# Performance work log

Measured on AMD Instinct MI355X. Metric: run time of the kernel, lower is better.

Reference implementation:

```python
import jax, jax.numpy as jnp
import numpy as np

B, S, H = 2, 2048, 1024
NH, HD = 16, 64
WINDOW = 512
NEG = -10000.0


def setup_inputs() -> dict:
    key = jax.random.key(0)
    ks = jax.random.split(key, 8)
    sc = 0.02
    return {
        "hidden_states": jax.random.normal(ks[0], (B, S, H), dtype=jnp.float32),
        "attention_mask": jnp.zeros((B, 1, 1, S), dtype=jnp.float32),
        "Wq": jax.random.normal(ks[1], (H, H), dtype=jnp.float32) * sc,
        "bq": jnp.zeros((H,), dtype=jnp.float32),
        "Wk": jax.random.normal(ks[2], (H, H), dtype=jnp.float32) * sc,
        "bk": jnp.zeros((H,), dtype=jnp.float32),
        "Wv": jax.random.normal(ks[3], (H, H), dtype=jnp.float32) * sc,
        "bv": jnp.zeros((H,), dtype=jnp.float32),
    }


def _heads(x):
    # [b, t, (h d)] -> [b, h, t, d]
    b, t, _ = x.shape
    return x.reshape(b, t, NH, HD).transpose(0, 2, 1, 3)


def reference(hidden_states, attention_mask, Wq, bq, Wk, bk, Wv, bv):
    q = _heads(hidden_states @ Wq.T + bq)
    k = _heads(hidden_states @ Wk.T + bk)
    v = _heads(hidden_states @ Wv.T + bv)

    # Faithful mask construction (note: window mask is triu(diag=-WINDOW),
    # penalizing the recent window, exactly as in the source).
    i = jnp.arange(S)[:, None]
    j = jnp.arange(S)[None, :]
    causal_mask = jnp.where(j > i, NEG, 0.0).astype(jnp.float32)          # triu, diag=1
    window_mask = jnp.where(j >= i - WINDOW, NEG, 0.0).astype(jnp.float32)  # triu, diag=-512
    mask = causal_mask + window_mask + attention_mask  # [b,1,S,S]

    scale = 1.0 / jnp.sqrt(jnp.asarray(HD, dtype=q.dtype))
    scores = jnp.einsum("bhtd,bhsd->bhts", q, k) * scale + mask  # [b,h,S,S]
    probs = jax.nn.softmax(scores, axis=-1)
    out = jnp.einsum("bhts,bhsd->bhtd", probs, v)  # [b,h,S,d]
    # [b,h,t,d] -> [b,t,(h d)]
    return out.transpose(0, 2, 1, 3).reshape(B, S, H)
```

## Files before the change

### kernel.cpp

```cpp
#include <hip/hip_runtime.h>

typedef float f32x2 __attribute__((ext_vector_type(2)));
typedef float f32x4 __attribute__((ext_vector_type(4)));
typedef float f32x16 __attribute__((ext_vector_type(16)));
typedef _Float16 half8 __attribute__((ext_vector_type(8)));
typedef _Float16 half4 __attribute__((ext_vector_type(4)));
typedef unsigned int u32;
typedef u32 u32x4 __attribute__((ext_vector_type(4)));

#define S_LEN 2048
#define NHEAD 16
#define HDIM 64
#define BATCH 2
#define WINDOW 512
#define M2_FIX 5.770780163555852f
#define LOG2E 1.4426950408889634f

#define GLDS16(gp, lp) __builtin_amdgcn_global_load_lds( \
    (const __attribute__((address_space(1))) void*)(gp), \
    (__attribute__((address_space(3))) void*)(lp), 16, 0, 0)


__global__ __launch_bounds__(256) void convert_kernel(
    const float4* __restrict__ hs, const float4* __restrict__ wq,
    const float4* __restrict__ wk, const float4* __restrict__ wv,
    _Float16* __restrict__ hsb, _Float16* __restrict__ wb) {
  int i = blockIdx.x * 256 + threadIdx.x;
  float4 v;
  _Float16* dst;
  if (i < 1048576) {
    v = hs[i];
    dst = hsb + (size_t)i * 4;
  } else {
    int j = i - 1048576;
    if (j < 262144) v = wq[j];
    else if (j < 524288) v = wk[j - 262144];
    else v = wv[j - 524288];
    dst = wb + (size_t)j * 4;
  }
  half4 o;
  o[0] = (_Float16)v.x; o[1] = (_Float16)v.y;
  o[2] = (_Float16)v.z; o[3] = (_Float16)v.w;
  *(half4*)dst = o;
}

__global__ __launch_bounds__(512) void qkv_gemm(
    const _Float16* __restrict__ A, const _Float16* __restrict__ W,
    const float* __restrict__ bq, const float* __restrict__ bk,
    const float* __restrict__ bv,
    _Float16* __restrict__ Qf, _Float16* __restrict__ Kf, _Float16* __restrict__ Vf) {
  __shared__ _Float16 sbuf[2][24576];
  const int tid = threadIdx.x;
  const int wv = tid >> 6;
  const int lane = tid & 63;
  const int g = lane >> 4;
  const int c = lane & 15;
  const int b = blockIdx.x;
  const int xcd = b & 7;
  const int s = b >> 3;
  const int m0 = ((xcd >> 2) * 8 + (s & 7)) * 256;
  const int n0 = ((xcd & 3) * 6 + (s >> 3)) * 128;
  const int wm = (wv & 3) * 64;
  const int wn = (wv >> 2) * 64;
  const _Float16* Asb0;
  const _Float16* Bsb0;

  const int srow8 = lane >> 3;
  const int sslot = lane & 7;
  const int lsl = sslot ^ srow8;
  const _Float16* aS = A + (size_t)(m0 + wv * 32 + srow8) * 1024 + lsl * 8;
  const _Float16* bS = W + (size_t)(n0 + wv * 16 + srow8) * 1024 + lsl * 8;
  const int aBase = wv * 2048;
  const int bBase = 16384 + wv * 1024;

  f32x4 acc[4][4];
#pragma unroll
  for (int i = 0; i < 4; ++i)
#pragma unroll
    for (int j = 0; j < 4; ++j) acc[i][j] = (f32x4){0.f, 0.f, 0.f, 0.f};

  auto STAGE = [&](int bf_, int k0) __attribute__((always_inline)) {
    char* aD = (char*)&sbuf[bf_][aBase];
    char* bD = (char*)&sbuf[bf_][bBase];
#pragma unroll
    for (int grp = 0; grp < 4; ++grp)
      GLDS16(aS + grp * 8192 + k0, aD + grp * 1024);
#pragma unroll
    for (int grp = 0; grp < 2; ++grp)
      GLDS16(bS + grp * 8192 + k0, bD + grp * 1024);
  };

  STAGE(0, 0);
  __syncthreads();
  int cur = 0;

  for (int t = 0; t < 16; ++t) {
    if (t < 15) STAGE(cur ^ 1, (t + 1) * 64);
    const _Float16* Asb = &sbuf[cur][0];
    const _Float16* Bsb = &sbuf[cur][16384];
    half8 af[4][2];
#pragma unroll
    for (int mf = 0; mf < 4; ++mf) {
      const int row = wm + mf * 16 + c;
#pragma unroll
      for (int ch = 0; ch < 2; ++ch)
        af[mf][ch] = *(const half8*)&Asb[row * 64 + ((ch * 4 + g) ^ (c & 7)) * 8];
    }
#pragma unroll
    for (int nf = 0; nf < 4; ++nf) {
      const int row = wn + nf * 16 + c;
      half8 bf0 = *(const half8*)&Bsb[row * 64 + ((g) ^ (c & 7)) * 8];
      half8 bf1 = *(const half8*)&Bsb[row * 64 + ((4 + g) ^ (c & 7)) * 8];
#pragma unroll
      for (int mf = 0; mf < 4; ++mf) {
        acc[mf][nf] = __builtin_amdgcn_mfma_f32_16x16x32_f16(af[mf][0], bf0, acc[mf][nf], 0, 0, 0);
        acc[mf][nf] = __builtin_amdgcn_mfma_f32_16x16x32_f16(af[mf][1], bf1, acc[mf][nf], 0, 0, 0);
      }
    }
    __syncthreads();
    cur ^= 1;
  }

  const int kind = n0 >> 10;
  const int nb = (n0 + wn) & 1023;
  const int head = nb >> 6;
  const float* bias = kind == 0 ? bq : (kind == 1 ? bk : bv);
  _Float16* dst = kind == 0 ? Qf : (kind == 1 ? Kf : Vf);
  _Float16* ob = &sbuf[0][0] + wv * 4096;

  if (kind < 2) {
    const float scl = kind == 0 ? (0.125f * LOG2E) : 1.0f;
#pragma unroll
    for (int nf = 0; nf < 4; ++nf) {
      const int d = nf * 16 + c;
      const float bsv = bias[nb + d];
      const int base = nf * 512 + ((c >> 3) & 1) * 256 + (c & 7);
#pragma unroll
      for (int mf = 0; mf < 4; ++mf) {
#pragma unroll
        for (int r = 0; r < 4; ++r) {
          ob[(mf >> 1) * 2048 + base + (mf & 1) * 128 + g * 32 + r * 8] =
              (_Float16)((acc[mf][nf][r] + bsv) * scl);
        }
      }
    }
  } else {
#pragma unroll
    for (int nf = 0; nf < 4; ++nf) {
      const int d = nf * 16 + c;
      const float bsv = bias[nb + d];
#pragma unroll
      for (int mf = 0; mf < 4; ++mf) {
        half4 v4;
#pragma unroll
        for (int r = 0; r < 4; ++r) v4[r] = (_Float16)(acc[mf][nf][r] + bsv);
        *(half4*)&ob[(mf >> 1) * 2048 + ((nf >> 1) * 2 + (mf & 1)) * 512 +
                     ((g >> 1) * 32 + (nf & 1) * 16 + c) * 8 + (g & 1) * 4] = v4;
      }
    }
  }

  const int bI = (m0 + wm) >> 11;
  const size_t gbase = (size_t)(bI * NHEAD + head) * 131072 +
                       (size_t)(((m0 + wm) & 2047) >> 5) * 2048;
#pragma unroll
  for (int i = 0; i < 8; ++i) {
    half8 v = *(const half8*)&ob[i * 512 + lane * 8];
    *(half8*)&dst[gbase + i * 512 + lane * 8] = v;
  }
}

__global__ __launch_bounds__(256) void attn_kernel(
    const _Float16* __restrict__ Qf, const _Float16* __restrict__ Kf,
    const _Float16* __restrict__ Vf, const float* __restrict__ amask,
    float* __restrict__ out) {
  __shared__ _Float16 obuf[4][32][72];
  __shared__ float lbuf[4][32];
  const int tid = threadIdx.x;
  const int w = tid >> 6;
  const int lane = tid & 63;
  const int q31 = lane & 31;
  const int h = lane >> 5;
  const int bid = blockIdx.x;
  const int bh = bid & 31;
  const int idx = 63 - (bid >> 5);
  const int i0 = idx * 32;
  const int bI = bh >> 4;
  const int head = bh & 15;

  const _Float16* Qh = Qf + (size_t)bh * 131072;
  const _Float16* Kh = Kf + (size_t)bh * 131072;
  const _Float16* Vh = Vf + (size_t)bh * 131072;
  const float* am = amask + (size_t)bI * S_LEN;

  const int q = i0 + q31;
  const int hiq = (q <= WINDOW) ? q : (q - WINDOW - 1);
  const int last = i0 + 31;
  const int himax = (last <= WINDOW) ? last
                    : ((i0 <= WINDOW) ? WINDOW : (last - WINDOW - 1));
  const int hiq_min = (last <= WINDOW) ? i0
                      : ((i0 > WINDOW) ? (i0 - WINDOW - 1) : 0);
  const int ntiles = (himax >> 5) + 1;
  const int nfull = (hiq_min + 1) >> 5;
  const int lim = hiq - 4 * h;

  half8 qf[4];
#pragma unroll
  for (int ch = 0; ch < 4; ++ch)
    qf[ch] = *(const half8*)&Qh[(size_t)idx * 2048 + ch * 512 + lane * 8];

  f32x16 zero16, m2init;
#pragma unroll
  for (int r = 0; r < 16; ++r) { zero16[r] = 0.f; m2init[r] = -M2_FIX; }
  f32x16 oacc0 = zero16, oacc1 = zero16;
  f32x2 lp[4];
#pragma unroll
  for (int r = 0; r < 4; ++r) lp[r] = (f32x2){0.f, 0.f};

  auto computeTile = [&](half8 k0, half8 k1, half8 k2, half8 k3,
                         half8 vf0, half8 vf1, half8 vf2, half8 vf3,
                         f32x4 am0, f32x4 am1, f32x4 am2, f32x4 am3, int t)
      __attribute__((always_inline)) {
    const int j0 = t * 32;
    f32x4 amv[4] = {am0, am1, am2, am3};

    __builtin_amdgcn_s_setprio(1);
    f32x16 st = __builtin_amdgcn_mfma_f32_32x32x16_f16(k0, qf[0], m2init, 0, 0, 0);
    st = __builtin_amdgcn_mfma_f32_32x32x16_f16(k1, qf[1], st, 0, 0, 0);
    st = __builtin_amdgcn_mfma_f32_32x32x16_f16(k2, qf[2], st, 0, 0, 0);
    st = __builtin_amdgcn_mfma_f32_32x32x16_f16(k3, qf[3], st, 0, 0, 0);
    __builtin_amdgcn_s_setprio(0);

    float p[16];
#pragma unroll
    for (int r = 0; r < 16; ++r)
      p[r] = __builtin_fmaf(amv[r >> 2][r & 3], LOG2E, st[r]);
    if (t >= nfull) {
      const int lm = lim - j0;
#pragma unroll
      for (int r = 0; r < 16; ++r) {
        const int off = (r & 3) + 8 * (r >> 2);
        p[r] = (off <= lm) ? p[r] : -3e38f;
      }
    }
#pragma unroll
    for (int r = 0; r < 16; ++r) p[r] = __builtin_amdgcn_exp2f(p[r]);
#pragma unroll
    for (int j = 0; j < 4; ++j) {
      lp[j] += (f32x2){p[2 * j], p[2 * j + 1]};
      lp[j] += (f32x2){p[8 + 2 * j], p[9 + 2 * j]};
    }

    u32 pk[8];
#pragma unroll
    for (int r = 0; r < 8; ++r) {
      auto c2 = __builtin_amdgcn_cvt_pkrtz(p[2 * r], p[2 * r + 1]);
      pk[r] = __builtin_bit_cast(u32, c2);
    }
    u32 a0 = pk[0], b0 = pk[2];
    u32 a1 = pk[1], b1 = pk[3];
    u32 a2 = pk[4], b2 = pk[6];
    u32 a3 = pk[5], b3 = pk[7];
    asm("v_permlane32_swap_b32 %0, %1" : "+v"(a0), "+v"(b0));
    asm("v_permlane32_swap_b32 %0, %1" : "+v"(a1), "+v"(b1));
    asm("v_permlane32_swap_b32 %0, %1" : "+v"(a2), "+v"(b2));
    asm("v_permlane32_swap_b32 %0, %1" : "+v"(a3), "+v"(b3));
    const half8 pf0 = __builtin_bit_cast(half8, (u32x4){a0, a1, b0, b1});
    const half8 pf1 = __builtin_bit_cast(half8, (u32x4){a2, a3, b2, b3});

    __builtin_amdgcn_s_setprio(1);
    oacc0 = __builtin_amdgcn_mfma_f32_32x32x16_f16(vf0, pf0, oacc0, 0, 0, 0);
    oacc0 = __builtin_amdgcn_mfma_f32_32x32x16_f16(vf1, pf1, oacc0, 0, 0, 0);
    oacc1 = __builtin_amdgcn_mfma_f32_32x32x16_f16(vf2, pf0, oacc1, 0, 0, 0);
    oacc1 = __builtin_amdgcn_mfma_f32_32x32x16_f16(vf3, pf1, oacc1, 0, 0, 0);
    __builtin_amdgcn_s_setprio(0);
  };

#define LOADALL(k0, k1, k2, k3, v0, v1, v2, v3, a0_, a1_, a2_, a3_, tt)  \
  {                                                                      \
    const _Float16* kt = Kh + (size_t)(tt) * 2048 + lane * 8;            \
    const _Float16* vt = Vh + (size_t)(tt) * 2048 + lane * 8;            \
    const float* at = am + (tt) * 32 + 4 * h;                            \
    k0 = *(const half8*)&kt[0];                                          \
    k1 = *(const half8*)&kt[512];                                        \
    k2 = *(const half8*)&kt[1024];                                       \
    k3 = *(const half8*)&kt[1536];                                       \
    v0 = *(const half8*)&vt[0];                                          \
    v1 = *(const half8*)&vt[512];                                        \
    v2 = *(const half8*)&vt[1024];                                       \
    v3 = *(const half8*)&vt[1536];                                       \
    a0_ = *(const f32x4*)&at[0];                                         \
    a1_ = *(const f32x4*)&at[8];                                         \
    a2_ = *(const f32x4*)&at[16];                                        \
    a3_ = *(const f32x4*)&at[24];                                        \
  }

  int t = w;
  if (t < ntiles) {
    half8 k0, k1, k2, k3, v0, v1, v2, v3;
    f32x4 a0, a1, a2, a3;
    LOADALL(k0, k1, k2, k3, v0, v1, v2, v3, a0, a1, a2, a3, t);
    int tn = t + 4;
    while (tn < ntiles) {
      half8 n0, n1, n2, n3, u0, u1, u2, u3;
      f32x4 e0, e1, e2, e3;
      LOADALL(n0, n1, n2, n3, u0, u1, u2, u3, e0, e1, e2, e3, tn);
      computeTile(k0, k1, k2, k3, v0, v1, v2, v3, a0, a1, a2, a3, t);
      k0 = n0; k1 = n1; k2 = n2; k3 = n3;
      v0 = u0; v1 = u1; v2 = u2; v3 = u3;
      a0 = e0; a1 = e1; a2 = e2; a3 = e3;
      t = tn;
      tn += 4;
    }
    computeTile(k0, k1, k2, k3, v0, v1, v2, v3, a0, a1, a2, a3, t);
  }

  f32x2 s2 = (lp[0] + lp[1]) + (lp[2] + lp[3]);
  float lw = s2[0] + s2[1];
  lw += __shfl_xor(lw, 32);
  if (h == 0) lbuf[w][q31] = lw;
#pragma unroll
  for (int j = 0; j < 4; ++j) {
    half4 h0, h1;
#pragma unroll
    for (int e = 0; e < 4; ++e) {
      h0[e] = (_Float16)oacc0[4 * j + e];
      h1[e] = (_Float16)oacc1[4 * j + e];
    }
    *(half4*)&obuf[w][q31][4 * h + 8 * j]      = h0;
    *(half4*)&obuf[w][q31][32 + 4 * h + 8 * j] = h1;
  }
  __syncthreads();

  const int mq = tid >> 3;
  const int md = (tid & 7) * 8;
  const float lt = (lbuf[0][mq] + lbuf[1][mq]) + (lbuf[2][mq] + lbuf[3][mq]);
  float s[8];
  half8 p0 = *(const half8*)&obuf[0][mq][md];
#pragma unroll
  for (int e = 0; e < 8; ++e) s[e] = (float)p0[e];
#pragma unroll
  for (int w4 = 1; w4 < 4; ++w4) {
    half8 pw = *(const half8*)&obuf[w4][mq][md];
#pragma unroll
    for (int e = 0; e < 8; ++e) s[e] += (float)pw[e];
  }
  const float inv = 1.0f / lt;
  float4 s0, s1;
  s0.x = s[0] * inv; s0.y = s[1] * inv; s0.z = s[2] * inv; s0.w = s[3] * inv;
  s1.x = s[4] * inv; s1.y = s[5] * inv; s1.z = s[6] * inv; s1.w = s[7] * inv;
  float* op = out + ((size_t)(bI * S_LEN + i0 + mq)) * 1024 + head * 64 + md;
  *(float4*)op = s0;
  *(float4*)(op + 4) = s1;
}

extern "C" void kernel_launch(void* const* d_in, const int* in_sizes, int n_in,
                              void* d_out, int out_size, void* d_ws, size_t ws_size,
                              hipStream_t stream) {
  const float* hs = (const float*)d_in[0];
  const float* am = (const float*)d_in[1];
  const float* Wq = (const float*)d_in[2];
  const float* bq = (const float*)d_in[3];
  const float* Wk = (const float*)d_in[4];
  const float* bk = (const float*)d_in[5];
  const float* Wv = (const float*)d_in[6];
  const float* bv = (const float*)d_in[7];
  float* out = (float*)d_out;

  char* ws = (char*)d_ws;
  _Float16* hsb = (_Float16*)(ws);
  _Float16* wb  = (_Float16*)(ws + 8388608);
  _Float16* Qf  = (_Float16*)(ws + 14680064);
  _Float16* Kf  = (_Float16*)(ws + 23068672);
  _Float16* Vf  = (_Float16*)(ws + 31457280);

  convert_kernel<<<7168, 256, 0, stream>>>(
      (const float4*)hs, (const float4*)Wq, (const float4*)Wk, (const float4*)Wv, hsb, wb);
  qkv_gemm<<<384, 512, 0, stream>>>(hsb, wb, bq, bk, bv, Qf, Kf, Vf);
  attn_kernel<<<2048, 256, 0, stream>>>(Qf, Kf, Vf, am, out);
}
```

Measured before the change: 78.05 us.

## Pre-swizzle operands into MFMA fragment layout and load GEMM fragments directly from global

The fp16 conversion kernel now writes hidden states and weights in a tiled layout that matches the MFMA 16x16x32 fragment order. The QKV GEMM then reads fragments straight from global memory into registers, double-buffered in registers, instead of staging through LDS with async global-to-LDS copies and barriers. Tiles shrink to 128x128 with 256 threads and 768 blocks. This removes LDS traffic and synchronisation, but relies on L2/cache reuse because each wave fetches its own operands from global memory.

Measured after the change: 105.9 us. +35.7%, slower.

```diff
diff --git a/kernel.cpp b/kernel.cpp
--- a/kernel.cpp
+++ b/kernel.cpp
@@ -16,40 +16,46 @@
 #define M2_FIX 5.770780163555852f
 #define LOG2E 1.4426950408889634f
 
-#define GLDS16(gp, lp) __builtin_amdgcn_global_load_lds( \
-    (const __attribute__((address_space(1))) void*)(gp), \
-    (__attribute__((address_space(3))) void*)(lp), 16, 0, 0)
-
 
 __global__ __launch_bounds__(256) void convert_kernel(
     const float4* __restrict__ hs, const float4* __restrict__ wq,
     const float4* __restrict__ wk, const float4* __restrict__ wv,
-    _Float16* __restrict__ hsb, _Float16* __restrict__ wb) {
+    _Float16* __restrict__ Af, _Float16* __restrict__ Wf) {
   int i = blockIdx.x * 256 + threadIdx.x;
   float4 v;
   _Float16* dst;
+  size_t off;
   if (i < 1048576) {
     v = hs[i];
-    dst = hsb + (size_t)i * 4;
+    const int m = i >> 8;
+    const int k = (i * 4) & 1023;
+    off = (size_t)(m >> 4) * 16384 + (k >> 6) * 1024 + ((k >> 5) & 1) * 512 +
+          ((k >> 3) & 3) * 128 + (m & 15) * 8 + (k & 7);
+    dst = Af;
   } else {
     int j = i - 1048576;
-    if (j < 262144) v = wq[j];
-    else if (j < 524288) v = wk[j - 262144];
-    else v = wv[j - 524288];
-    dst = wb + (size_t)j * 4;
+    int kind;
+    if (j < 262144) { v = wq[j]; kind = 0; }
+    else if (j < 524288) { v = wk[j - 262144]; kind = 1; j -= 262144; }
+    else { v = wv[j - 524288]; kind = 2; j -= 524288; }
+    const int n = (j >> 8) + (kind << 10);
+    const int k = (j * 4) & 1023;
+    off = (size_t)(n >> 4) * 16384 + (k >> 6) * 1024 + ((k >> 5) & 1) * 512 +
+          ((k >> 3) & 3) * 128 + (n & 15) * 8 + (k & 7);
+    dst = Wf;
   }
   half4 o;
   o[0] = (_Float16)v.x; o[1] = (_Float16)v.y;
   o[2] = (_Float16)v.z; o[3] = (_Float16)v.w;
-  *(half4*)dst = o;
+  *(half4*)&dst[off] = o;
 }
 
-__global__ __launch_bounds__(512) void qkv_gemm(
-    const _Float16* __restrict__ A, const _Float16* __restrict__ W,
+__global__ __launch_bounds__(256) void qkv_gemm(
+    const _Float16* __restrict__ Af, const _Float16* __restrict__ Wf,
     const float* __restrict__ bq, const float* __restrict__ bk,
     const float* __restrict__ bv,
     _Float16* __restrict__ Qf, _Float16* __restrict__ Kf, _Float16* __restrict__ Vf) {
-  __shared__ _Float16 sbuf[2][24576];
+  __shared__ _Float16 ob4[16384];
   const int tid = threadIdx.x;
   const int wv = tid >> 6;
   const int lane = tid & 63;
@@ -58,20 +64,15 @@
   const int b = blockIdx.x;
   const int xcd = b & 7;
   const int s = b >> 3;
-  const int m0 = ((xcd >> 2) * 8 + (s & 7)) * 256;
-  const int n0 = ((xcd & 3) * 6 + (s >> 3)) * 128;
-  const int wm = (wv & 3) * 64;
-  const int wn = (wv >> 2) * 64;
-  const _Float16* Asb0;
-  const _Float16* Bsb0;
-
-  const int srow8 = lane >> 3;
-  const int sslot = lane & 7;
-  const int lsl = sslot ^ srow8;
-  const _Float16* aS = A + (size_t)(m0 + wv * 32 + srow8) * 1024 + lsl * 8;
-  const _Float16* bS = W + (size_t)(n0 + wv * 16 + srow8) * 1024 + lsl * 8;
-  const int aBase = wv * 2048;
-  const int bBase = 16384 + wv * 1024;
+  const int sub = s / 48;
+  const int rem = s - sub * 48;
+  const int m0 = (((xcd >> 1) << 3) + rem / 6) * 128;
+  const int n0 = ((xcd & 1) * 12 + sub * 6 + rem % 6) * 128;
+  const int wm = (wv & 1) * 64;
+  const int wn = (wv >> 1) * 64;
+
+  const _Float16* aP = Af + (size_t)((m0 + wm) >> 4) * 16384 + lane * 8;
+  const _Float16* bP = Wf + (size_t)((n0 + wn) >> 4) * 16384 + lane * 8;
 
   f32x4 acc[4][4];
 #pragma unroll
@@ -79,46 +80,32 @@
 #pragma unroll
     for (int j = 0; j < 4; ++j) acc[i][j] = (f32x4){0.f, 0.f, 0.f, 0.f};
 
-  auto STAGE = [&](int bf_, int k0) __attribute__((always_inline)) {
-    char* aD = (char*)&sbuf[bf_][aBase];
-    char* bD = (char*)&sbuf[bf_][bBase];
-#pragma unroll
-    for (int grp = 0; grp < 4; ++grp)
-      GLDS16(aS + grp * 8192 + k0, aD + grp * 1024);
-#pragma unroll
-    for (int grp = 0; grp < 2; ++grp)
-      GLDS16(bS + grp * 8192 + k0, bD + grp * 1024);
-  };
-
-  STAGE(0, 0);
-  __syncthreads();
-  int cur = 0;
-
-  for (int t = 0; t < 16; ++t) {
-    if (t < 15) STAGE(cur ^ 1, (t + 1) * 64);
-    const _Float16* Asb = &sbuf[cur][0];
-    const _Float16* Bsb = &sbuf[cur][16384];
-    half8 af[4][2];
-#pragma unroll
-    for (int mf = 0; mf < 4; ++mf) {
-      const int row = wm + mf * 16 + c;
-#pragma unroll
-      for (int ch = 0; ch < 2; ++ch)
-        af[mf][ch] = *(const half8*)&Asb[row * 64 + ((ch * 4 + g) ^ (c & 7)) * 8];
-    }
-#pragma unroll
-    for (int nf = 0; nf < 4; ++nf) {
-      const int row = wn + nf * 16 + c;
-      half8 bf0 = *(const half8*)&Bsb[row * 64 + ((g) ^ (c & 7)) * 8];
-      half8 bf1 = *(const half8*)&Bsb[row * 64 + ((4 + g) ^ (c & 7)) * 8];
-#pragma unroll
-      for (int mf = 0; mf < 4; ++mf) {
-        acc[mf][nf] = __builtin_amdgcn_mfma_f32_16x16x32_f16(af[mf][0], bf0, acc[mf][nf], 0, 0, 0);
-        acc[mf][nf] = __builtin_amdgcn_mfma_f32_16x16x32_f16(af[mf][1], bf1, acc[mf][nf], 0, 0, 0);
-      }
-    }
-    __syncthreads();
-    cur ^= 1;
+#define LDT(dA, dB, t)                                                        \
+  {                                                                           \
+    _Pragma("unroll") for (int mf = 0; mf < 4; ++mf)                          \
+        _Pragma("unroll") for (int ch = 0; ch < 2; ++ch) {                    \
+      dA[mf][ch] = *(const half8*)&aP[mf * 16384 + (t) * 1024 + ch * 512];    \
+      dB[mf][ch] = *(const half8*)&bP[mf * 16384 + (t) * 1024 + ch * 512];    \
+    }                                                                         \
+  }
+#define CMP(sA, sB)                                                           \
+  {                                                                           \
+    _Pragma("unroll") for (int nf = 0; nf < 4; ++nf)                          \
+        _Pragma("unroll") for (int mf = 0; mf < 4; ++mf) {                    \
+      acc[mf][nf] = __builtin_amdgcn_mfma_f32_16x16x32_f16(                   \
+          sA[mf][0], sB[nf][0], acc[mf][nf], 0, 0, 0);                        \
+      acc[mf][nf] = __builtin_amdgcn_mfma_f32_16x16x32_f16(                   \
+          sA[mf][1], sB[nf][1], acc[mf][nf], 0, 0, 0);                        \
+    }                                                                         \
+  }
+
+  half8 afA[4][2], bfA[4][2], afB[4][2], bfB[4][2];
+  LDT(afA, bfA, 0);
+  for (int t = 0; t < 16; t += 2) {
+    if (t + 1 < 16) LDT(afB, bfB, t + 1);
+    CMP(afA, bfA);
+    if (t + 2 < 16) LDT(afA, bfA, t + 2);
+    CMP(afB, bfB);
   }
 
   const int kind = n0 >> 10;
@@ -126,7 +113,7 @@
   const int head = nb >> 6;
   const float* bias = kind == 0 ? bq : (kind == 1 ? bk : bv);
   _Float16* dst = kind == 0 ? Qf : (kind == 1 ? Kf : Vf);
-  _Float16* ob = &sbuf[0][0] + wv * 4096;
+  _Float16* ob = ob4 + wv * 4096;
 
   if (kind < 2) {
     const float scl = kind == 0 ? (0.125f * LOG2E) : 1.0f;
@@ -368,14 +355,14 @@
   float* out = (float*)d_out;
 
   char* ws = (char*)d_ws;
-  _Float16* hsb = (_Float16*)(ws);
-  _Float16* wb  = (_Float16*)(ws + 8388608);
+  _Float16* Af  = (_Float16*)(ws);
+  _Float16* Wfb = (_Float16*)(ws + 8388608);
   _Float16* Qf  = (_Float16*)(ws + 14680064);
   _Float16* Kf  = (_Float16*)(ws + 23068672);
   _Float16* Vf  = (_Float16*)(ws + 31457280);
 
   convert_kernel<<<7168, 256, 0, stream>>>(
-      (const float4*)hs, (const float4*)Wq, (const float4*)Wk, (const float4*)Wv, hsb, wb);
-  qkv_gemm<<<384, 512, 0, stream>>>(hsb, wb, bq, bk, bv, Qf, Kf, Vf);
+      (const float4*)hs, (const float4*)Wq, (const float4*)Wk, (const float4*)Wv, Af, Wfb);
+  qkv_gemm<<<768, 256, 0, stream>>>(Af, Wfb, bq, bk, bv, Qf, Kf, Vf);
   attn_kernel<<<2048, 256, 0, stream>>>(Qf, Kf, Vf, am, out);
 }
```
